# Optimization experiments

Measured on AMD Instinct MI355X. Metric: run time of the kernel, lower is better.

The kernel has to match this reference:

```python
import jax, jax.numpy as jnp
import numpy as np

N = 100000; D = 256; ATT = 512; H = 8; HD = ATT // H; E = 250000
TYPE_CT = 64; TS = 64; P = 8192; PC = 1024; MP = 131072; MC = 16384


def setup_inputs() -> dict:
    key = jax.random.key(0)
    ks = jax.random.split(key, 24)
    sD = 1.0 / np.sqrt(D); sT = 1.0 / np.sqrt(TS); sA = 1.0 / np.sqrt(ATT); sC = 1.0 / np.sqrt(D + ATT)
    inp = {}
    inp['node_states'] = jax.random.normal(ks[0], (N, D), jnp.float32)
    inp['node_types'] = jax.random.randint(ks[1], (N,), 0, TYPE_CT, jnp.int32)
    inp['pair_conj'] = jax.random.randint(ks[2], (E,), 0, N, jnp.int32)
    inp['pair_prem'] = jax.random.randint(ks[3], (E,), 0, N, jnp.int32)
    inp['pool_prem_nodes'] = jax.random.randint(ks[4], (MP,), 0, N, jnp.int32)
    inp['pool_prem_seg'] = ((jnp.arange(MP, dtype=jnp.int32) * P) // MP).astype(jnp.int32)  # every prem set non-empty
    inp['pool_conj_nodes'] = jax.random.randint(ks[5], (MC,), 0, N, jnp.int32)
    inp['pool_conj_seg'] = ((jnp.arange(MC, dtype=jnp.int32) * PC) // MC).astype(jnp.int32)
    inp['prem2conj'] = jax.random.randint(ks[6], (P,), 0, PC, jnp.int32)
    # learned parameters
    inp['ln_g'] = jnp.ones((D,), jnp.float32)
    inp['ln_b'] = jnp.zeros((D,), jnp.float32)
    inp['emb_p'] = jax.random.normal(ks[7], (TYPE_CT, TS), jnp.float32) * 0.02
    inp['wp_w'] = jax.random.normal(ks[8], (TS, ATT), jnp.float32) * sT
    inp['wp_b'] = jnp.zeros((ATT,), jnp.float32)
    inp['emb_c'] = jax.random.normal(ks[9], (TYPE_CT, TS), jnp.float32) * 0.02
    inp['wc_w'] = jax.random.normal(ks[10], (TS, ATT), jnp.float32) * sT
    inp['wc_b'] = jnp.zeros((ATT,), jnp.float32)
    inp['Wq_p'] = jax.random.normal(ks[11], (H, D, HD), jnp.float32) * sD
    inp['Wk_p'] = jax.random.normal(ks[12], (H, D, HD), jnp.float32) * sD
    inp['Wv_p'] = jax.random.normal(ks[13], (H, D, HD), jnp.float32) * sD
    inp['Wo_p'] = jax.random.normal(ks[14], (ATT, ATT), jnp.float32) * sA
    inp['Wq_c'] = jax.random.normal(ks[15], (H, D, HD), jnp.float32) * sD
    inp['Wk_c'] = jax.random.normal(ks[16], (H, D, HD), jnp.float32) * sD
    inp['Wv_c'] = jax.random.normal(ks[17], (H, D, HD), jnp.float32) * sD
    inp['Wo_c'] = jax.random.normal(ks[18], (ATT, ATT), jnp.float32) * sA
    inp['W_dag'] = jax.random.normal(ks[19], (D + ATT, D + ATT), jnp.float32) * sC
    inp['b_dag'] = jnp.zeros((D + ATT,), jnp.float32)
    return inp


def _layernorm(x, g, b):
    mu = jnp.mean(x, axis=-1, keepdims=True)
    var = jnp.mean(jnp.square(x - mu), axis=-1, keepdims=True)
    return (x - mu) * jax.lax.rsqrt(var + 1e-5) * g + b


def _mha_dir(x, src, tgt, Wq, Wk, Wv, Wo, gate):
    # gather query/key/value node reprs along the pair list (irregular gather)
    xs = x[src]; xt = x[tgt]                       # [E, D]
    q = jnp.einsum('ed,hdk->ehk', xs, Wq)          # [E, H, HD]
    k = jnp.einsum('ed,hdk->ehk', xt, Wk)
    scores = jnp.sum(q * k, axis=-1) / np.sqrt(HD)  # [E, H]
    # per-query-node (segment) softmax, as in compute_att_aggr grouping
    m = jax.ops.segment_max(scores, src, num_segments=N)
    ex = jnp.exp(scores - m[src])
    denom = jax.ops.segment_sum(ex, src, num_segments=N)
    prob = ex / denom[src]
    v = jnp.einsum('ed,hdk->ehk', xt, Wv)
    # adj_matr @ comb_matr scatter-aggregation
    agg = jax.ops.segment_sum(prob[..., None] * v, src, num_segments=N)  # [N, H, HD]
    return gate * (agg.reshape(N, H * HD) @ Wo)


def reference(node_states, node_types, pair_conj, pair_prem, pool_prem_nodes, pool_prem_seg,
              pool_conj_nodes, pool_conj_seg, prem2conj,
              ln_g, ln_b, emb_p, wp_w, wp_b, emb_c, wc_w, wc_b,
              Wq_p, Wk_p, Wv_p, Wo_p, Wq_c, Wk_c, Wv_c, Wo_c, W_dag, b_dag):
    x = _layernorm(node_states, ln_g, ln_b)                                  # ne_norm(node reprs)
    gate_p = jax.nn.sigmoid(emb_p[node_types] @ wp_w + wp_b)                 # prem_gate  [N, ATT]
    gate_c = jax.nn.sigmoid(emb_c[node_types] @ wc_w + wc_b)                 # conj_gate
    # just_prem pairs: (prem, conj) -> query/scatter node = prem, key/value node = conj
    comb = _mha_dir(x, pair_prem, pair_conj, Wq_p, Wk_p, Wv_p, Wo_p, gate_p)
    # just_conj pairs: (conj, prem)
    comb = comb + _mha_dir(x, pair_conj, pair_prem, Wq_c, Wk_c, Wv_c, Wo_c, gate_c)
    h = jnp.concatenate([x, comb], axis=1)                                   # [N, D+ATT]
    pooled = jnp.tanh(h @ W_dag + b_dag)                                     # simplified dag_lstm pass
    prem_r = jax.ops.segment_max(pooled[pool_prem_nodes], pool_prem_seg, num_segments=P)
    conj_sets = jax.ops.segment_max(pooled[pool_conj_nodes], pool_conj_seg, num_segments=PC)
    conj_r = conj_sets[prem2conj]
    return jnp.concatenate([prem_r, conj_r], axis=1)                         # [P, 2*(D+ATT)]
```

## Files before the change

kernel.cpp:

```cpp
#include <hip/hip_runtime.h>
#include <math.h>

#define N_NODES 100000
#define DIM 256
#define ATT 512
#define NH 8
#define HD 64
#define E_PAIRS 250000
#define TYPE_CT 64
#define TS 64
#define P_SEG 8192
#define PC_SEG 1024
#define MP_SZ 131072
#define MC_SZ 16384
#define CD 768

typedef unsigned short u16;
typedef __attribute__((ext_vector_type(8))) short short8v;
typedef __attribute__((ext_vector_type(4))) float floatx4;

__device__ __forceinline__ u16 f2b(float f) {
    unsigned u = __float_as_uint(f);
    return (u16)((u + 0x7FFFu + ((u >> 16) & 1u)) >> 16);
}
__device__ __forceinline__ float b2f(u16 h) {
    return __uint_as_float(((unsigned)h) << 16);
}

template<int N>
__device__ __forceinline__ void waitcnt_vm() {
    asm volatile("s_waitcnt vmcnt(%0)" :: "n"(N) : "memory");
}
__device__ __forceinline__ void barrier_fence() {
    asm volatile("s_barrier" ::: "memory");
    __builtin_amdgcn_sched_barrier(0);
}

__device__ __forceinline__ void remap8(int flat, int gx, int& bx, int& by) {
    int yc = flat & 7;
    int t = flat >> 3;
    bx = t % gx;
    by = yc + 8 * (t / gx);
}

__global__ __launch_bounds__(256) void fill_val_k(float* out, int n, float v) {
    int i = blockIdx.x * 256 + threadIdx.x;
    if (i < n) out[i] = v;
}

__global__ __launch_bounds__(64) void layernorm_k(
    const float* __restrict__ ns, const float* __restrict__ g,
    const float* __restrict__ b, u16* __restrict__ x)
{
    int row = blockIdx.x;
    int lane = threadIdx.x;
    float4 v = ((const float4*)(ns + (size_t)row * DIM))[lane];
    float sum = v.x + v.y + v.z + v.w;
    #pragma unroll
    for (int off = 32; off >= 1; off >>= 1) sum += __shfl_xor(sum, off);
    float mu = sum * (1.0f / DIM);
    float dx = v.x - mu, dy = v.y - mu, dz = v.z - mu, dw = v.w - mu;
    float sq = dx * dx + dy * dy + dz * dz + dw * dw;
    #pragma unroll
    for (int off = 32; off >= 1; off >>= 1) sq += __shfl_xor(sq, off);
    float rs = rsqrtf(sq * (1.0f / DIM) + 1e-5f);
    float4 gg = ((const float4*)g)[lane];
    float4 bb = ((const float4*)b)[lane];
    u16 o4[4];
    o4[0] = f2b(dx * rs * gg.x + bb.x);
    o4[1] = f2b(dy * rs * gg.y + bb.y);
    o4[2] = f2b(dz * rs * gg.z + bb.z);
    o4[3] = f2b(dw * rs * gg.w + bb.w);
    *(uint2*)(x + (size_t)row * DIM + lane * 4) = *(uint2*)o4;
}

__global__ __launch_bounds__(512) void gate_table_k(
    const float* __restrict__ emb, const float* __restrict__ w,
    const float* __restrict__ wb, float* __restrict__ tab)
{
    int t = blockIdx.x;
    int a = threadIdx.x;
    float acc = wb[a];
    #pragma unroll 8
    for (int s = 0; s < TS; ++s) acc += emb[t * TS + s] * w[s * ATT + a];
    tab[t * ATT + a] = 1.0f / (1.0f + expf(-acc));
}

__global__ __launch_bounds__(256) void wcvt_k(
    const float* __restrict__ W, u16* __restrict__ Bt, int K, int N)
{
    int idx = blockIdx.x * 256 + threadIdx.x;
    if (idx >= K * N) return;
    int c = idx / K, k = idx - c * K;
    Bt[idx] = f2b(W[(size_t)k * N + c]);
}

__global__ __launch_bounds__(256) void wqkv_cvt_k(
    const float* __restrict__ Wq, const float* __restrict__ Wk,
    const float* __restrict__ Wv, u16* __restrict__ outp)
{
    int idx = blockIdx.x * 256 + threadIdx.x;
    if (idx >= NH * 3 * HD * DIM) return;
    int k = idx & (DIM - 1);
    int c = (idx >> 8) & (HD - 1);
    int hm = idx >> 14;
    int m = hm % 3;
    int h = hm / 3;
    const float* W = (m == 0) ? Wq : ((m == 1) ? Wk : Wv);
    outp[idx] = f2b(W[((size_t)h * DIM + k) * HD + c]);
}

template<int BM, int WN, int DEPTH, int EPI>
__device__ __forceinline__ void gemm_body3(
    int bm, int bn,
    const u16* __restrict__ A, int lda,
    const u16* __restrict__ A2, int lda2, int K1,
    const u16* __restrict__ Bt, int ldb,
    u16* __restrict__ C, int ldc,
    int M, int K,
    const float* __restrict__ bias,
    const float* __restrict__ gateTab,
    const int* __restrict__ types)
{
    constexpr int BN = 32 * WN;
    constexpr int AR = BM / 64;
    constexpr int BR = BN / 64;
    constexpr int LA = AR + BR;
    constexpr int AF = BM / 32;
    __shared__ u16 As[DEPTH][BM * 32];
    __shared__ u16 Bs[DEPTH][BN * 32];
    const int tid = threadIdx.x;
    const int wave = tid >> 6, lane = tid & 63;
    const int wm = (wave >> 1) * (BM / 2), wn = (wave & 1) * 16 * WN;
    const int srow = tid >> 2;
    const int skk = (((tid & 3) ^ ((srow >> 1) & 3)) * 8);
    floatx4 acc[AF][WN] = {};

    auto stage = [&](int buf, int k0) {
        #pragma unroll
        for (int rnd = 0; rnd < AR; ++rnd) {
            int grow = bm + srow + rnd * 64;
            if (grow > M - 1) grow = M - 1;
            int gk = k0 + skk;
            const u16* src;
            if (EPI == 2 && gk >= K1) src = A2 + (size_t)grow * lda2 + (gk - K1);
            else                      src = A + (size_t)grow * lda + gk;
            __builtin_amdgcn_global_load_lds(
                (const __attribute__((address_space(1))) void*)src,
                (__attribute__((address_space(3))) void*)(&As[buf][rnd * 2048 + wave * 512]),
                16, 0, 0);
        }
        #pragma unroll
        for (int rnd = 0; rnd < BR; ++rnd) {
            const u16* src = Bt + (size_t)(bn + srow + rnd * 64) * ldb + k0 + skk;
            __builtin_amdgcn_global_load_lds(
                (const __attribute__((address_space(1))) void*)src,
                (__attribute__((address_space(3))) void*)(&Bs[buf][rnd * 2048 + wave * 512]),
                16, 0, 0);
        }
    };

    const int NS = K >> 5;
    #pragma unroll
    for (int p = 0; p < DEPTH - 1; ++p)
        if (p < NS) stage(p, p * 32);
    const int rr = lane & 15;
    const int cq = lane >> 4;
    int cur = 0;
    for (int is = 0; is < NS; ++is) {
        int pend = NS - 1 - is;
        if (pend > DEPTH - 2) pend = DEPTH - 2;
        if (pend >= 2)      waitcnt_vm<2 * LA>();
        else if (pend == 1) waitcnt_vm<LA>();
        else                waitcnt_vm<0>();
        barrier_fence();
        if (is + DEPTH - 1 < NS) stage((cur + DEPTH - 1) % DEPTH, (is + DEPTH - 1) * 32);
        short8v a[AF], b[WN];
        #pragma unroll
        for (int i = 0; i < AF; ++i) {
            int ar = wm + i * 16 + rr;
            a[i] = *(const short8v*)&As[cur][ar * 32 + ((cq ^ ((ar >> 1) & 3)) * 8)];
        }
        #pragma unroll
        for (int j = 0; j < WN; ++j) {
            int br = wn + j * 16 + rr;
            b[j] = *(const short8v*)&Bs[cur][br * 32 + ((cq ^ ((br >> 1) & 3)) * 8)];
        }
        #pragma unroll
        for (int i = 0; i < AF; ++i)
            #pragma unroll
            for (int j = 0; j < WN; ++j)
                acc[i][j] = __builtin_amdgcn_mfma_f32_16x16x32_bf16(
                    a[i], b[j], acc[i][j], 0, 0, 0);
        cur = (cur + 1) % DEPTH;
    }
    #pragma unroll
    for (int i = 0; i < AF; ++i) {
        #pragma unroll
        for (int j = 0; j < WN; ++j) {
            #pragma unroll
            for (int q = 0; q < 4; ++q) {
                int row = bm + wm + i * 16 + (lane >> 4) * 4 + q;
                if (row >= M) continue;
                int col = bn + wn + j * 16 + (lane & 15);
                float v = acc[i][j][q];
                size_t idx = (size_t)row * ldc + col;
                if (EPI == 0) C[idx] = f2b(v);
                else if (EPI == 1) {
                    float g = gateTab[types[row] * ATT + col];
                    C[idx] = f2b(b2f(C[idx]) + g * v);
                } else if (EPI == 3) {
                    float g = gateTab[types[row] * ATT + col];
                    C[idx] = f2b(g * v);
                } else {
                    C[idx] = f2b(tanhf(v + bias[col]));
                }
            }
        }
    }
}

#define MB64 1563
#define MB64P 1568

__global__ __launch_bounds__(256) void gemm_qkv(
    const u16* __restrict__ A, const u16* __restrict__ Bt, u16* __restrict__ C)
{
    gemm_body3<64, 6, 3, 0>(blockIdx.y * 64, 0,
                            A, DIM, nullptr, 0, 1 << 30, Bt, DIM, C, 192,
                            N_NODES, DIM, nullptr, nullptr, nullptr);
}
__global__ __launch_bounds__(256) void gemm_wo_first(
    const u16* __restrict__ A, const u16* __restrict__ Bt, u16* __restrict__ C,
    const float* __restrict__ gateTab, const int* __restrict__ types)
{
    int bx, by; remap8(blockIdx.x, 4, bx, by);
    if (by >= MB64) return;
    gemm_body3<64, 4, 3, 3>(by * 64, bx * 128,
                            A, ATT, nullptr, 0, 1 << 30, Bt, ATT, C, ATT,
                            N_NODES, ATT, nullptr, gateTab, types);
}
__global__ __launch_bounds__(256) void gemm_wo_acc(
    const u16* __restrict__ A, const u16* __restrict__ Bt, u16* __restrict__ C,
    const float* __restrict__ gateTab, const int* __restrict__ types)
{
    int bx, by; remap8(blockIdx.x, 4, bx, by);
    if (by >= MB64) return;
    gemm_body3<64, 4, 3, 1>(by * 64, bx * 128,
                            A, ATT, nullptr, 0, 1 << 30, Bt, ATT, C, ATT,
                            N_NODES, ATT, nullptr, gateTab, types);
}
__global__ __launch_bounds__(256) void gemm_dag(
    const u16* __restrict__ A, const u16* __restrict__ A2,
    const u16* __restrict__ Bt, u16* __restrict__ C,
    const float* __restrict__ bias)
{
    int bx, by; remap8(blockIdx.x, 3, bx, by);
    if (by >= MB64) return;
    gemm_body3<64, 4, 3, 2>(by * 64, bx * 128,
                            A, DIM, A2, ATT, DIM, Bt, CD, C, 384,
                            N_NODES, CD, bias, nullptr, nullptr);
}

__global__ __launch_bounds__(256) void count_k(
    const int* __restrict__ src, int* __restrict__ counts)
{
    int e = blockIdx.x * 256 + threadIdx.x;
    if (e < E_PAIRS) atomicAdd(&counts[src[e]], 1);
}
__global__ __launch_bounds__(256) void scan1_k(
    const int* __restrict__ counts, int* __restrict__ offs, int* __restrict__ bsums)
{
    __shared__ int sm[256];
    int i = blockIdx.x * 256 + threadIdx.x;
    int v = (i < N_NODES) ? counts[i] : 0;
    sm[threadIdx.x] = v;
    __syncthreads();
    for (int d = 1; d < 256; d <<= 1) {
        int t = (threadIdx.x >= d) ? sm[threadIdx.x - d] : 0;
        __syncthreads();
        sm[threadIdx.x] += t;
        __syncthreads();
    }
    if (i < N_NODES) offs[i] = sm[threadIdx.x] - v;
    if (threadIdx.x == 255) bsums[blockIdx.x] = sm[255];
}
__global__ __launch_bounds__(512) void scan2_k(int* __restrict__ bsums, int nb)
{
    __shared__ int sm[512];
    int tx = threadIdx.x;
    int v = (tx < nb) ? bsums[tx] : 0;
    sm[tx] = v;
    __syncthreads();
    for (int d = 1; d < 512; d <<= 1) {
        int t = (tx >= d) ? sm[tx - d] : 0;
        __syncthreads();
        sm[tx] += t;
        __syncthreads();
    }
    if (tx < nb) bsums[tx] = sm[tx] - v;
}
__global__ __launch_bounds__(256) void addcur_k(
    int* __restrict__ offs, const int* __restrict__ bsums, int* __restrict__ cur)
{
    int i = blockIdx.x * 256 + threadIdx.x;
    if (i >= N_NODES) return;
    int o = offs[i] + bsums[i >> 8];
    offs[i] = o;
    cur[i] = o;
}
__global__ __launch_bounds__(256) void scatter_k(
    const int* __restrict__ src, const int* __restrict__ tgt,
    int* __restrict__ cur, int* __restrict__ csr_tgt)
{
    int e = blockIdx.x * 256 + threadIdx.x;
    if (e >= E_PAIRS) return;
    int p = atomicAdd(&cur[src[e]], 1);
    csr_tgt[p] = tgt[e];
}

__global__ __launch_bounds__(256) void attn_k(
    const u16* __restrict__ qkv, const int* __restrict__ offs,
    const int* __restrict__ counts, const int* __restrict__ csr_tgt,
    u16* __restrict__ agg, int h)
{
    int s = blockIdx.x * 4 + (threadIdx.x >> 6);
    if (s >= N_NODES) return;
    int lane = threadIdx.x & 63;
    float q = b2f(qkv[(size_t)s * 192 + lane]) * 0.125f;
    int lo = offs[s], deg = counts[s];
    float m = -INFINITY, l = 0.0f, acc = 0.0f;
    for (int i = 0; i < deg; ++i) {
        int t = csr_tgt[lo + i];
        float kd = b2f(qkv[(size_t)t * 192 + 64 + lane]);
        float vd = b2f(qkv[(size_t)t * 192 + 128 + lane]);
        float p = q * kd;
        #pragma unroll
        for (int off = 32; off >= 1; off >>= 1) p += __shfl_xor(p, off);
        float mn = fmaxf(m, p);
        float sc = expf(m - mn);
        float w  = expf(p - mn);
        l = l * sc + w;
        acc = acc * sc + w * vd;
        m = mn;
    }
    float r = (deg > 0) ? acc / l : 0.0f;
    agg[(size_t)s * ATT + h * HD + lane] = f2b(r);
}

template<int BFOUT>
__global__ __launch_bounds__(256) void seg_max_k(
    const u16* __restrict__ pooled, const int* __restrict__ nodes,
    const int* __restrict__ seg, int total, void* __restrict__ outv, int ldo)
{
    int p = blockIdx.x;
    int lo, hi;
    { int a = 0, b2 = total; while (a < b2) { int mid = (a + b2) >> 1; if (seg[mid] < p) a = mid + 1; else b2 = mid; } lo = a; }
    { int a = lo, b2 = total; while (a < b2) { int mid = (a + b2) >> 1; if (seg[mid] < p + 1) a = mid + 1; else b2 = mid; } hi = a; }
    for (int c = threadIdx.x; c < 384; c += 256) {
        float mx = -INFINITY;
        for (int i = lo; i < hi; ++i)
            mx = fmaxf(mx, b2f(pooled[(size_t)nodes[i] * 384 + c]));
        if (BFOUT) ((u16*)outv)[(size_t)p * ldo + c] = f2b(mx);
        else       ((float*)outv)[(size_t)p * ldo + c] = mx;
    }
}

__global__ __launch_bounds__(768) void gather_conj(
    const u16* __restrict__ cs, const int* __restrict__ p2c,
    float* __restrict__ out)
{
    int p = blockIdx.x;
    int c = threadIdx.x;
    out[(size_t)p * (2 * CD) + CD + c] = b2f(cs[(size_t)p2c[p] * CD + c]);
}

extern "C" void kernel_launch(void* const* d_in, const int* in_sizes, int n_in,
                              void* d_out, int out_size, void* d_ws, size_t ws_size,
                              hipStream_t stream) {
    const float* node_states     = (const float*)d_in[0];
    const int*   node_types      = (const int*)d_in[1];
    const int*   pair_conj       = (const int*)d_in[2];
    const int*   pair_prem       = (const int*)d_in[3];
    const int*   pool_prem_nodes = (const int*)d_in[4];
    const int*   pool_prem_seg   = (const int*)d_in[5];
    const int*   pool_conj_nodes = (const int*)d_in[6];
    const int*   pool_conj_seg   = (const int*)d_in[7];
    const int*   prem2conj       = (const int*)d_in[8];
    const float* ln_g  = (const float*)d_in[9];
    const float* ln_b  = (const float*)d_in[10];
    const float* emb_p = (const float*)d_in[11];
    const float* wp_w  = (const float*)d_in[12];
    const float* wp_b  = (const float*)d_in[13];
    const float* emb_c = (const float*)d_in[14];
    const float* wc_w  = (const float*)d_in[15];
    const float* wc_b  = (const float*)d_in[16];
    const float* Wq_p  = (const float*)d_in[17];
    const float* Wk_p  = (const float*)d_in[18];
    const float* Wv_p  = (const float*)d_in[19];
    const float* Wo_p  = (const float*)d_in[20];
    const float* Wq_c  = (const float*)d_in[21];
    const float* Wk_c  = (const float*)d_in[22];
    const float* Wv_c  = (const float*)d_in[23];
    const float* Wo_c  = (const float*)d_in[24];
    const float* W_dag = (const float*)d_in[25];
    const float* b_dag = (const float*)d_in[26];
    float* out = (float*)d_out;

    char* ws = (char*)d_ws;
    size_t o = 0;
    u16* x_bf  = (u16*)(ws + o); o += (size_t)N_NODES * DIM * 2;
    u16* comb  = (u16*)(ws + o); o += (size_t)N_NODES * ATT * 2;
    u16* R     = (u16*)(ws + o); o += (size_t)N_NODES * ATT * 2;
    char* csrb = ws + o;         o += 8000000;
    u16* conj_sets = (u16*)(ws + o); o += (size_t)PC_SEG * CD * 2;
    const size_t WS_NEEDED = o;

    if (ws_size < WS_NEEDED) {
        fill_val_k<<<(out_size + 255) / 256, 256, 0, stream>>>(out, out_size, (float)ws_size);
        return;
    }

    u16* agg    = R;
    u16* pooled = R;
    int* c_counts[2], *c_offs[2], *c_cur[2], *c_tgt[2];
    for (int d = 0; d < 2; ++d) {
        char* base = csrb + (size_t)d * 2200000;
        c_counts[d] = (int*)(base + 0);
        c_offs[d]   = (int*)(base + 400000);
        c_cur[d]    = (int*)(base + 800000);
        c_tgt[d]    = (int*)(base + 1200000);
    }
    int* bsums = (int*)(csrb + 4400000);
    u16* wdag_t = (u16*)csrb;

    char* ob = (char*)d_out;
    u16* qkv     = (u16*)(ob + 0);
    float* gtab_p = (float*)(ob + 38400000);
    float* gtab_c = (float*)(ob + 38531072);
    u16* wqkv_t  = (u16*)(ob + 38662144);
    u16* wo_t    = (u16*)(ob + 40235008);

    layernorm_k<<<N_NODES, 64, 0, stream>>>(node_states, ln_g, ln_b, x_bf);
    gate_table_k<<<TYPE_CT, ATT, 0, stream>>>(emb_p, wp_w, wp_b, gtab_p);
    gate_table_k<<<TYPE_CT, ATT, 0, stream>>>(emb_c, wc_w, wc_b, gtab_c);
    wqkv_cvt_k<<<(NH * 3 * HD * DIM + 255) / 256, 256, 0, stream>>>(
        Wq_p, Wk_p, Wv_p, wqkv_t);
    wqkv_cvt_k<<<(NH * 3 * HD * DIM + 255) / 256, 256, 0, stream>>>(
        Wq_c, Wk_c, Wv_c, wqkv_t + (size_t)NH * 3 * HD * DIM);
    wcvt_k<<<(ATT * ATT + 255) / 256, 256, 0, stream>>>(Wo_p, wo_t, ATT, ATT);
    wcvt_k<<<(ATT * ATT + 255) / 256, 256, 0, stream>>>(
        Wo_c, wo_t + (size_t)ATT * ATT, ATT, ATT);

    const int NSCAN = (N_NODES + 255) / 256;
    for (int d = 0; d < 2; ++d) {
        const int* src = d ? pair_conj : pair_prem;
        const int* tgt = d ? pair_prem : pair_conj;
        hipMemsetAsync(c_counts[d], 0, 400000, stream);
        count_k<<<(E_PAIRS + 255) / 256, 256, 0, stream>>>(src, c_counts[d]);
        scan1_k<<<NSCAN, 256, 0, stream>>>(c_counts[d], c_offs[d], bsums);
        scan2_k<<<1, 512, 0, stream>>>(bsums, NSCAN);
        addcur_k<<<NSCAN, 256, 0, stream>>>(c_offs[d], bsums, c_cur[d]);
        scatter_k<<<(E_PAIRS + 255) / 256, 256, 0, stream>>>(src, tgt, c_cur[d], c_tgt[d]);
    }

    for (int dir = 0; dir < 2; ++dir) {
        const float* gt = dir ? gtab_c : gtab_p;
        const u16* wq_d = wqkv_t + (size_t)dir * NH * 3 * HD * DIM;
        const u16* wo_d = wo_t + (size_t)dir * ATT * ATT;

        for (int h = 0; h < NH; ++h) {
            gemm_qkv<<<dim3(1, MB64), 256, 0, stream>>>(
                x_bf, wq_d + (size_t)h * 3 * HD * DIM, qkv);
            attn_k<<<(N_NODES + 3) / 4, 256, 0, stream>>>(
                qkv, c_offs[dir], c_counts[dir], c_tgt[dir], agg, h);
        }

        if (dir == 0)
            gemm_wo_first<<<4 * MB64P, 256, 0, stream>>>(
                agg, wo_d, comb, gt, node_types);
        else
            gemm_wo_acc<<<4 * MB64P, 256, 0, stream>>>(
                agg, wo_d, comb, gt, node_types);
    }

    wcvt_k<<<(CD * CD + 255) / 256, 256, 0, stream>>>(W_dag, wdag_t, CD, CD);

    for (int c0 = 0; c0 < CD; c0 += 384) {
        gemm_dag<<<3 * MB64P, 256, 0, stream>>>(
            x_bf, comb, wdag_t + (size_t)c0 * CD, pooled, b_dag + c0);
        seg_max_k<0><<<P_SEG, 256, 0, stream>>>(
            pooled, pool_prem_nodes, pool_prem_seg, MP_SZ, out + c0, 2 * CD);
        seg_max_k<1><<<PC_SEG, 256, 0, stream>>>(
            pooled, pool_conj_nodes, pool_conj_seg, MC_SZ, conj_sets + c0, CD);
    }
    gather_conj<<<P_SEG, CD, 0, stream>>>(conj_sets, prem2conj, out);
}
```

Baseline: 2.128 ms.

## Batch all-head QKV projection into one GEMM and prefetch neighbor K/V in attention

When the workspace is large enough, the per-head QKV GEMM and attention launches (8 each per direction) are replaced by one GEMM producing all heads' Q/K/V into a 1536-wide buffer and one attention launch with a head grid dimension. The attention loop also software-prefetches the next neighbor's K/V values before computing the current step, to hide gather latency. This needs about 300MB of extra workspace, and if that is unavailable it falls back to the old path. The wider rows reduce locality for the per-head K/V gathers.

```diff
diff --git a/kernel.cpp b/kernel.cpp
--- a/kernel.cpp
+++ b/kernel.cpp
@@ -230,6 +230,15 @@
                             A, DIM, nullptr, 0, 1 << 30, Bt, DIM, C, 192,
                             N_NODES, DIM, nullptr, nullptr, nullptr);
 }
+__global__ __launch_bounds__(256) void gemm_qkv_all(
+    const u16* __restrict__ A, const u16* __restrict__ Bt, u16* __restrict__ C)
+{
+    int bx, by; remap8(blockIdx.x, 8, bx, by);
+    if (by >= MB64) return;
+    gemm_body3<64, 6, 3, 0>(by * 64, bx * 192,
+                            A, DIM, nullptr, 0, 1 << 30, Bt, DIM, C, 1536,
+                            N_NODES, DIM, nullptr, nullptr, nullptr);
+}
 __global__ __launch_bounds__(256) void gemm_wo_first(
     const u16* __restrict__ A, const u16* __restrict__ Bt, u16* __restrict__ C,
     const float* __restrict__ gateTab, const int* __restrict__ types)
@@ -319,30 +328,42 @@
     csr_tgt[p] = tgt[e];
 }
 
+template<int MULTI>
 __global__ __launch_bounds__(256) void attn_k(
-    const u16* __restrict__ qkv, const int* __restrict__ offs,
-    const int* __restrict__ counts, const int* __restrict__ csr_tgt,
-    u16* __restrict__ agg, int h)
+    const u16* __restrict__ qkv, int ld,
+    const int* __restrict__ offs, const int* __restrict__ counts,
+    const int* __restrict__ csr_tgt, u16* __restrict__ agg, int h_in)
 {
     int s = blockIdx.x * 4 + (threadIdx.x >> 6);
     if (s >= N_NODES) return;
+    int h = MULTI ? blockIdx.y : h_in;
+    const u16* base = MULTI ? (qkv + h * 192) : qkv;
     int lane = threadIdx.x & 63;
-    float q = b2f(qkv[(size_t)s * 192 + lane]) * 0.125f;
+    float q = b2f(base[(size_t)s * ld + lane]) * 0.125f;
     int lo = offs[s], deg = counts[s];
     float m = -INFINITY, l = 0.0f, acc = 0.0f;
-    for (int i = 0; i < deg; ++i) {
-        int t = csr_tgt[lo + i];
-        float kd = b2f(qkv[(size_t)t * 192 + 64 + lane]);
-        float vd = b2f(qkv[(size_t)t * 192 + 128 + lane]);
-        float p = q * kd;
-        #pragma unroll
-        for (int off = 32; off >= 1; off >>= 1) p += __shfl_xor(p, off);
-        float mn = fmaxf(m, p);
-        float sc = expf(m - mn);
-        float w  = expf(p - mn);
-        l = l * sc + w;
-        acc = acc * sc + w * vd;
-        m = mn;
+    if (deg > 0) {
+        int t0 = csr_tgt[lo];
+        u16 kc = base[(size_t)t0 * ld + 64 + lane];
+        u16 vc = base[(size_t)t0 * ld + 128 + lane];
+        for (int i = 0; i < deg; ++i) {
+            u16 kn = 0, vn = 0;
+            if (i + 1 < deg) {
+                int tn = csr_tgt[lo + i + 1];
+                kn = base[(size_t)tn * ld + 64 + lane];
+                vn = base[(size_t)tn * ld + 128 + lane];
+            }
+            float p = q * b2f(kc);
+            #pragma unroll
+            for (int off = 32; off >= 1; off >>= 1) p += __shfl_xor(p, off);
+            float mn = fmaxf(m, p);
+            float sc = expf(m - mn);
+            float w  = expf(p - mn);
+            l = l * sc + w;
+            acc = acc * sc + w * b2f(vc);
+            m = mn;
+            kc = kn; vc = vn;
+        }
     }
     float r = (deg > 0) ? acc / l : 0.0f;
     agg[(size_t)s * ATT + h * HD + lane] = f2b(r);
@@ -420,6 +441,9 @@
         fill_val_k<<<(out_size + 255) / 256, 256, 0, stream>>>(out, out_size, (float)ws_size);
         return;
     }
+    u16* qkv_all = (u16*)(ws + WS_NEEDED);
+    const size_t BIG_NEEDED = WS_NEEDED + (size_t)N_NODES * 1536 * 2;
+    const bool big = (ws_size >= BIG_NEEDED);
 
     u16* agg    = R;
     u16* pooled = R;
@@ -469,11 +493,17 @@
         const u16* wq_d = wqkv_t + (size_t)dir * NH * 3 * HD * DIM;
         const u16* wo_d = wo_t + (size_t)dir * ATT * ATT;
 
-        for (int h = 0; h < NH; ++h) {
-            gemm_qkv<<<dim3(1, MB64), 256, 0, stream>>>(
-                x_bf, wq_d + (size_t)h * 3 * HD * DIM, qkv);
-            attn_k<<<(N_NODES + 3) / 4, 256, 0, stream>>>(
-                qkv, c_offs[dir], c_counts[dir], c_tgt[dir], agg, h);
+        if (big) {
+            gemm_qkv_all<<<8 * MB64P, 256, 0, stream>>>(x_bf, wq_d, qkv_all);
+            attn_k<1><<<dim3((N_NODES + 3) / 4, NH), 256, 0, stream>>>(
+                qkv_all, 1536, c_offs[dir], c_counts[dir], c_tgt[dir], agg, 0);
+        } else {
+            for (int h = 0; h < NH; ++h) {
+                gemm_qkv<<<dim3(1, MB64), 256, 0, stream>>>(
+                    x_bf, wq_d + (size_t)h * 3 * HD * DIM, qkv);
+                attn_k<0><<<(N_NODES + 3) / 4, 256, 0, stream>>>(
+                    qkv, 192, c_offs[dir], c_counts[dir], c_tgt[dir], agg, h);
+            }
         }
 
         if (dir == 0)
```

New measurement: 2.127 ms. About the same (-0.0%).
